# Performance work log

Measured on AMD Instinct MI355X. Metric: run time of the kernel, lower is better.

Reference implementation:

```python
import jax, jax.numpy as jnp
import numpy as np

NUM_HEADS = 16
HEAD_DIM = 64  # d_model // num_heads = 1024 // 16
NUM_BUCKETS = 20


def setup_inputs() -> dict:
    key = jax.random.key(0)
    ks = jax.random.split(key, 5)
    B, S, D = 2, 2048, 1024
    v = jax.random.normal(ks[0], (B, S, D), dtype=jnp.float32)
    k = jax.random.normal(ks[1], (B, S, D), dtype=jnp.float32)
    q = jax.random.normal(ks[2], (B, S, D), dtype=jnp.float32)
    mask = jax.random.randint(ks[3], (B, S, S), 0, 2).astype(jnp.bool_)
    diff_matrix = jax.random.randint(ks[4], (B, S, S), 0, NUM_BUCKETS)
    rel_bias = jax.random.normal(jax.random.fold_in(key, 7), (NUM_BUCKETS, NUM_HEADS), dtype=jnp.float32)
    return {"v": v, "k": k, "q": q, "mask": mask, "diff_matrix": diff_matrix, "rel_bias": rel_bias}


def _split_heads(x):
    B, S, _ = x.shape
    return x.reshape(B, S, NUM_HEADS, HEAD_DIM).transpose(0, 2, 1, 3)  # [B,H,S,hd]


def reference(v, k, q, mask, diff_matrix, rel_bias):
    B, S, D = q.shape
    qh, kh, vh = _split_heads(q), _split_heads(k), _split_heads(v)
    scale = 1.0 / jnp.sqrt(jnp.float32(HEAD_DIM))
    scores = jnp.einsum('bhqd,bhkd->bhqk', qh, kh) * scale  # [B,H,S,S]
    # relative bias: gather [B,S,S,H] -> [B,H,S,S]
    bias = rel_bias[diff_matrix].transpose(0, 3, 1, 2)
    att = jax.nn.silu(scores + bias)
    att = jnp.where(mask[:, None, :, :], att, 0.0)
    av = jnp.einsum('bhqk,bhkd->bhqd', att, vh)  # [B,H,S,hd]
    return av.transpose(0, 2, 1, 3).reshape(B, S, D)
```

## Files before the change

### kernel.cpp

```cpp
#include <hip/hip_runtime.h>
#include <cstdint>
#include <cstddef>

#define SEQ 2048
#define DM 1024
#define NH 16
#define NB 20

typedef _Float16 half8 __attribute__((ext_vector_type(8)));
typedef _Float16 half4 __attribute__((ext_vector_type(4)));
typedef float f32x4 __attribute__((ext_vector_type(4)));
typedef int i32x4 __attribute__((ext_vector_type(4)));
typedef unsigned int u32;
typedef unsigned int u32x2 __attribute__((ext_vector_type(2)));

#define KF_HALVES 4194304
#define VF_HALVES 4194304

__global__ __launch_bounds__(256) void pa_prep(
    const float* __restrict__ v, const float* __restrict__ k,
    const int* __restrict__ diff, const int* __restrict__ mask,
    _Float16* __restrict__ KF, _Float16* __restrict__ VF,
    unsigned char* __restrict__ PB) {
  const int bid = blockIdx.x, tid = threadIdx.x;
  if (bid < 2048) {
    int img = bid >> 4;
    int bb = img >> 6, kt = img & 63;
    int tix = ((bid & 15) << 8) | tid;
    int r = tix >> 7;
    int c0 = (tix & 127) << 3;
    const float* src = k + ((size_t)(bb * SEQ + kt * 32 + r)) * DM + c0;
    f32x4 a = *(const f32x4*)src;
    f32x4 c = *(const f32x4*)(src + 4);
    half8 o = {(_Float16)a[0], (_Float16)a[1], (_Float16)a[2], (_Float16)a[3],
               (_Float16)c[0], (_Float16)c[1], (_Float16)c[2], (_Float16)c[3]};
    int h = c0 >> 6, dh = (c0 >> 5) & 1, g4 = (c0 >> 3) & 3;
    int k2 = r >> 4, l16 = r & 15;
    int lane = g4 * 16 + l16;
    size_t off = ((size_t)((bb * 16 + h) * 64 + kt)) * 2048 + (k2 * 2 + dh) * 512 + lane * 8;
    *(half8*)(KF + off) = o;
  } else if (bid < 3072) {
    int b3 = bid - 2048;
    int img = b3 >> 3;
    int bb = img >> 6, kt = img & 63;
    int tix = ((b3 & 7) << 8) | tid;
    int kq = tix >> 8;
    int k2 = kq >> 2, g4 = kq & 3;
    int d0 = (tix & 255) << 2;
    const float* src = v + ((size_t)(bb * SEQ + kt * 32 + k2 * 16 + g4 * 4)) * DM + d0;
    f32x4 m0 = *(const f32x4*)(src);
    f32x4 m1 = *(const f32x4*)(src + DM);
    f32x4 m2 = *(const f32x4*)(src + 2 * DM);
    f32x4 m3 = *(const f32x4*)(src + 3 * DM);
#pragma unroll
    for (int i = 0; i < 4; ++i) {
      int d = d0 + i;
      int l16 = d & 15, dt = (d >> 4) & 3, dtp = dt >> 1, w = dt & 1, h = d >> 6;
      int lane = g4 * 16 + l16;
      half4 o = {(_Float16)m0[i], (_Float16)m1[i], (_Float16)m2[i], (_Float16)m3[i]};
      size_t off = ((size_t)((bb * 16 + h) * 64 + kt)) * 2048 + (k2 * 2 + dtp) * 512 + lane * 8 + w * 4;
      *(half4*)(VF + off) = o;
    }
  } else {
    int b4 = bid - 3072;
    int job = b4 >> 5;
    int bb = job >> 6, qblk = job & 63;
    int tix = ((b4 & 31) << 8) | tid;
    int kt = tix >> 7;
    int rem = tix & 127;
    int g4 = rem & 3, l16 = (rem >> 2) & 15, qs = rem >> 6;
    int lane = g4 * 16 + l16;
    int qrow = qblk * 32 + qs * 16 + l16;
    size_t rowbase = ((size_t)(bb * SEQ + qrow)) * SEQ;
    u32x2 wds;
#pragma unroll
    for (int k2 = 0; k2 < 2; ++k2) {
      int kk = kt * 32 + k2 * 16 + g4 * 4;
      i32x4 dv = *(const i32x4*)(diff + rowbase + kk);
      i32x4 mv = *(const i32x4*)(mask + rowbase + kk);
      u32 wd = 0;
#pragma unroll
      for (int r = 0; r < 4; ++r) {
        u32 byte = mv[r] ? (u32)dv[r] : 20u;
        wd |= byte << (8 * r);
      }
      wds[k2] = wd;
    }
    size_t off = ((size_t)job) * 65536 + (size_t)(kt * 2 + qs) * 512 + lane * 8;
    *(u32x2*)(PB + off) = wds;
  }
}

__global__ __launch_bounds__(256, 4) void pa_main(
    const _Float16* __restrict__ KF, const _Float16* __restrict__ VF,
    const unsigned char* __restrict__ PB, const float* __restrict__ q,
    const float* __restrict__ relbias, float* __restrict__ out) {
  const int tid = threadIdx.x, lane = tid & 63, wid = tid >> 6;
  const int l16 = lane & 15, g4 = lane >> 4;
  const int bid = blockIdx.x;
  const int g = bid & 7;
  const int b = g >> 2, ksp = (g >> 1) & 1, hh = g & 1;
  const int rid = bid >> 3;
  const int qblk = rid & 63, hq = rid >> 6;
  const int h = hh * 8 + hq * 4 + wid;
  const int qbase = qblk * 32;

  float rbv = -30000.f;
  if (lane < NB) rbv = relbias[lane * NH + h];
  const int rbi = __float_as_int(rbv);

  half8 qf[2][2];
#pragma unroll
  for (int qs = 0; qs < 2; ++qs)
#pragma unroll
    for (int dh = 0; dh < 2; ++dh) {
      const float* s = q + ((size_t)(b * SEQ + qbase + qs * 16 + l16)) * DM + h * 64 + dh * 32 + g4 * 8;
      f32x4 a = *(const f32x4*)s;
      f32x4 c = *(const f32x4*)(s + 4);
      qf[qs][dh] = {(_Float16)a[0], (_Float16)a[1], (_Float16)a[2], (_Float16)a[3],
                    (_Float16)c[0], (_Float16)c[1], (_Float16)c[2], (_Float16)c[3]};
    }

  const f32x4 zf = {0.f, 0.f, 0.f, 0.f};
  f32x4 acc[2][4];
#pragma unroll
  for (int qs = 0; qs < 2; ++qs)
#pragma unroll
    for (int dt = 0; dt < 4; ++dt) acc[qs][dt] = zf;

  const _Float16* kfb = KF + ((size_t)((b * 16 + h) * 64 + ksp * 32)) * 2048 + lane * 8;
  const _Float16* vfb = VF + ((size_t)((b * 16 + h) * 64 + ksp * 32)) * 2048 + lane * 8;
  const unsigned char* pbb = PB + ((size_t)(b * 64 + qblk)) * 65536 + (size_t)(ksp * 32) * 1024 + lane * 8;

  for (int t = 0; t < 32; ++t) {
    half8 kf[2][2], vv[2][2];
#pragma unroll
    for (int k2 = 0; k2 < 2; ++k2)
#pragma unroll
      for (int j = 0; j < 2; ++j) {
        kf[k2][j] = *(const half8*)(kfb + (k2 * 2 + j) * 512);
        vv[k2][j] = *(const half8*)(vfb + (k2 * 2 + j) * 512);
      }
    u32x2 pbw[2];
    pbw[0] = *(const u32x2*)(pbb);
    pbw[1] = *(const u32x2*)(pbb + 512);

#pragma unroll
    for (int k2 = 0; k2 < 2; ++k2) {
      f32x4 sa[2];
#pragma unroll
      for (int qs = 0; qs < 2; ++qs) {
        sa[qs] = __builtin_amdgcn_mfma_f32_16x16x32_f16(kf[k2][0], qf[qs][0], zf, 0, 0, 0);
        sa[qs] = __builtin_amdgcn_mfma_f32_16x16x32_f16(kf[k2][1], qf[qs][1], sa[qs], 0, 0, 0);
      }
      half4 pf[2];
#pragma unroll
      for (int qs = 0; qs < 2; ++qs) {
        u32 u = pbw[qs][k2];
#pragma unroll
        for (int r = 0; r < 4; ++r) {
          int idx = (int)(((u >> (8 * r)) & 0xffu) << 2);
          float bias = __int_as_float(__builtin_amdgcn_ds_bpermute(idx, rbi));
          float x = fmaf(sa[qs][r], 0.125f, bias);
          float e = __expf(-x);
          float y = x * __builtin_amdgcn_rcpf(1.0f + e);
          pf[qs][r] = (_Float16)y;
        }
      }
      half4 vf0 = __builtin_shufflevector(vv[k2][0], vv[k2][0], 0, 1, 2, 3);
      half4 vf1 = __builtin_shufflevector(vv[k2][0], vv[k2][0], 4, 5, 6, 7);
      half4 vf2 = __builtin_shufflevector(vv[k2][1], vv[k2][1], 0, 1, 2, 3);
      half4 vf3 = __builtin_shufflevector(vv[k2][1], vv[k2][1], 4, 5, 6, 7);
#pragma unroll
      for (int qs = 0; qs < 2; ++qs) {
        acc[qs][0] = __builtin_amdgcn_mfma_f32_16x16x16f16(pf[qs], vf0, acc[qs][0], 0, 0, 0);
        acc[qs][1] = __builtin_amdgcn_mfma_f32_16x16x16f16(pf[qs], vf1, acc[qs][1], 0, 0, 0);
        acc[qs][2] = __builtin_amdgcn_mfma_f32_16x16x16f16(pf[qs], vf2, acc[qs][2], 0, 0, 0);
        acc[qs][3] = __builtin_amdgcn_mfma_f32_16x16x16f16(pf[qs], vf3, acc[qs][3], 0, 0, 0);
      }
    }
    kfb += 2048; vfb += 2048; pbb += 1024;
  }

#pragma unroll
  for (int qs = 0; qs < 2; ++qs)
#pragma unroll
    for (int dt = 0; dt < 4; ++dt)
#pragma unroll
      for (int r = 0; r < 4; ++r) {
        int qrow = qbase + qs * 16 + g4 * 4 + r;
        int d = h * 64 + dt * 16 + l16;
        atomicAdd(&out[((size_t)(b * SEQ) + qrow) * DM + d], acc[qs][dt][r]);
      }
}

extern "C" void kernel_launch(void* const* d_in, const int* in_sizes, int n_in,
                              void* d_out, int out_size, void* d_ws, size_t ws_size,
                              hipStream_t stream) {
  const float* v = (const float*)d_in[0];
  const float* k = (const float*)d_in[1];
  const float* q = (const float*)d_in[2];
  const int* mask = (const int*)d_in[3];
  const int* diff = (const int*)d_in[4];
  const float* relbias = (const float*)d_in[5];
  float* out = (float*)d_out;

  _Float16* KF = (_Float16*)d_ws;
  _Float16* VF = KF + KF_HALVES;
  unsigned char* PB = (unsigned char*)(VF + VF_HALVES);
  if (ws_size < (size_t)25165824) return;

  hipMemsetAsync(d_out, 0, (size_t)out_size * sizeof(float), stream);
  pa_prep<<<7168, 256, 0, stream>>>(v, k, diff, mask, KF, VF, PB);
  pa_main<<<1024, 256, 0, stream>>>(KF, VF, PB, q, relbias, out);
}
```

Before: 108.3 us.

## Compute SiLU in packed fp16, fold scale into Q, remap blocks and pack bias bytes

The SiLU epilogue now runs in packed half2 arithmetic (exp2, rcp) instead of per-element fp32 expf and rcp. The 1/8 score scale is folded into Q at load time, and the bias indices are pre-shifted in the prep kernel so the lane-permute needs no shift. The bias-byte layout is changed so each lane loads 16 bytes in one access. Blocks are remapped so the four waves in a block share a head and work on different query blocks, improving K/V reuse across waves, and the loop is unrolled by 2. The fp16 SiLU loses precision and can overflow or underflow for large scores.

```diff
diff --git a/kernel.cpp b/kernel.cpp
--- a/kernel.cpp
+++ b/kernel.cpp
@@ -1,4 +1,5 @@
 #include <hip/hip_runtime.h>
+#include <hip/hip_fp16.h>
 #include <cstdint>
 #include <cstddef>
 
@@ -9,6 +10,7 @@
 
 typedef _Float16 half8 __attribute__((ext_vector_type(8)));
 typedef _Float16 half4 __attribute__((ext_vector_type(4)));
+typedef _Float16 h2v __attribute__((ext_vector_type(2)));
 typedef float f32x4 __attribute__((ext_vector_type(4)));
 typedef int i32x4 __attribute__((ext_vector_type(4)));
 typedef unsigned int u32;
@@ -81,14 +83,34 @@
       u32 wd = 0;
 #pragma unroll
       for (int r = 0; r < 4; ++r) {
-        u32 byte = mv[r] ? (u32)dv[r] : 20u;
+        u32 byte = mv[r] ? ((u32)dv[r] << 2) : 80u;
         wd |= byte << (8 * r);
       }
       wds[k2] = wd;
     }
-    size_t off = ((size_t)job) * 65536 + (size_t)(kt * 2 + qs) * 512 + lane * 8;
+    size_t off = ((size_t)job) * 65536 + (size_t)kt * 1024 + (size_t)lane * 16 + (size_t)qs * 8;
     *(u32x2*)(PB + off) = wds;
   }
+}
+
+__device__ __forceinline__ half4 silu4(const f32x4& s, u32 u, int rbi) {
+  float b0 = __int_as_float(__builtin_amdgcn_ds_bpermute((int)(u & 0xffu), rbi));
+  float b1 = __int_as_float(__builtin_amdgcn_ds_bpermute((int)((u >> 8) & 0xffu), rbi));
+  float b2 = __int_as_float(__builtin_amdgcn_ds_bpermute((int)((u >> 16) & 0xffu), rbi));
+  float b3 = __int_as_float(__builtin_amdgcn_ds_bpermute((int)(u >> 24), rbi));
+  h2v x01 = __builtin_bit_cast(h2v, __builtin_amdgcn_cvt_pkrtz(s[0], s[1])) +
+            __builtin_bit_cast(h2v, __builtin_amdgcn_cvt_pkrtz(b0, b1));
+  h2v x23 = __builtin_bit_cast(h2v, __builtin_amdgcn_cvt_pkrtz(s[2], s[3])) +
+            __builtin_bit_cast(h2v, __builtin_amdgcn_cvt_pkrtz(b2, b3));
+  const h2v NL2E = {(_Float16)-1.44269504f, (_Float16)-1.44269504f};
+  const h2v ONE = {(_Float16)1.0f, (_Float16)1.0f};
+  h2v m01 = x01 * NL2E, m23 = x23 * NL2E;
+  h2v e01 = __builtin_bit_cast(h2v, h2exp2(__builtin_bit_cast(__half2, m01)));
+  h2v e23 = __builtin_bit_cast(h2v, h2exp2(__builtin_bit_cast(__half2, m23)));
+  h2v d01 = e01 + ONE, d23 = e23 + ONE;
+  h2v y01 = x01 * __builtin_bit_cast(h2v, h2rcp(__builtin_bit_cast(__half2, d01)));
+  h2v y23 = x23 * __builtin_bit_cast(h2v, h2rcp(__builtin_bit_cast(__half2, d23)));
+  return (half4){y01[0], y01[1], y23[0], y23[1]};
 }
 
 __global__ __launch_bounds__(256, 4) void pa_main(
@@ -97,16 +119,15 @@
     const float* __restrict__ relbias, float* __restrict__ out) {
   const int tid = threadIdx.x, lane = tid & 63, wid = tid >> 6;
   const int l16 = lane & 15, g4 = lane >> 4;
-  const int bid = blockIdx.x;
-  const int g = bid & 7;
-  const int b = g >> 2, ksp = (g >> 1) & 1, hh = g & 1;
-  const int rid = bid >> 3;
-  const int qblk = rid & 63, hq = rid >> 6;
-  const int h = hh * 8 + hq * 4 + wid;
+  const int L = (blockIdx.x & 7) * 128 + (blockIdx.x >> 3);
+  const int h = L & 15;
+  const int qgrp = (L >> 4) & 15;
+  const int ksp = (L >> 8) & 1;
+  const int b = L >> 9;
+  const int qblk = qgrp * 4 + wid;
   const int qbase = qblk * 32;
 
-  float rbv = -30000.f;
-  if (lane < NB) rbv = relbias[lane * NH + h];
+  const float rbv = (lane < NB) ? relbias[lane * NH + h] : -30000.0f;
   const int rbi = __float_as_int(rbv);
 
   half8 qf[2][2];
@@ -117,8 +138,10 @@
       const float* s = q + ((size_t)(b * SEQ + qbase + qs * 16 + l16)) * DM + h * 64 + dh * 32 + g4 * 8;
       f32x4 a = *(const f32x4*)s;
       f32x4 c = *(const f32x4*)(s + 4);
-      qf[qs][dh] = {(_Float16)a[0], (_Float16)a[1], (_Float16)a[2], (_Float16)a[3],
-                    (_Float16)c[0], (_Float16)c[1], (_Float16)c[2], (_Float16)c[3]};
+      qf[qs][dh] = {(_Float16)(a[0] * 0.125f), (_Float16)(a[1] * 0.125f),
+                    (_Float16)(a[2] * 0.125f), (_Float16)(a[3] * 0.125f),
+                    (_Float16)(c[0] * 0.125f), (_Float16)(c[1] * 0.125f),
+                    (_Float16)(c[2] * 0.125f), (_Float16)(c[3] * 0.125f)};
     }
 
   const f32x4 zf = {0.f, 0.f, 0.f, 0.f};
@@ -130,47 +153,34 @@
 
   const _Float16* kfb = KF + ((size_t)((b * 16 + h) * 64 + ksp * 32)) * 2048 + lane * 8;
   const _Float16* vfb = VF + ((size_t)((b * 16 + h) * 64 + ksp * 32)) * 2048 + lane * 8;
-  const unsigned char* pbb = PB + ((size_t)(b * 64 + qblk)) * 65536 + (size_t)(ksp * 32) * 1024 + lane * 8;
-
+  const unsigned char* pbb = PB + ((size_t)(b * 64 + qblk)) * 65536 + (size_t)(ksp * 32) * 1024 + lane * 16;
+
+#pragma unroll 2
   for (int t = 0; t < 32; ++t) {
-    half8 kf[2][2], vv[2][2];
-#pragma unroll
-    for (int k2 = 0; k2 < 2; ++k2)
-#pragma unroll
-      for (int j = 0; j < 2; ++j) {
-        kf[k2][j] = *(const half8*)(kfb + (k2 * 2 + j) * 512);
-        vv[k2][j] = *(const half8*)(vfb + (k2 * 2 + j) * 512);
-      }
-    u32x2 pbw[2];
-    pbw[0] = *(const u32x2*)(pbb);
-    pbw[1] = *(const u32x2*)(pbb + 512);
+    half8 kfr[4], vvr[4];
+#pragma unroll
+    for (int j = 0; j < 4; ++j) {
+      kfr[j] = *(const half8*)(kfb + (size_t)t * 2048 + j * 512);
+      vvr[j] = *(const half8*)(vfb + (size_t)t * 2048 + j * 512);
+    }
+    i32x4 pq = *(const i32x4*)(pbb + (size_t)t * 1024);
 
 #pragma unroll
     for (int k2 = 0; k2 < 2; ++k2) {
       f32x4 sa[2];
 #pragma unroll
       for (int qs = 0; qs < 2; ++qs) {
-        sa[qs] = __builtin_amdgcn_mfma_f32_16x16x32_f16(kf[k2][0], qf[qs][0], zf, 0, 0, 0);
-        sa[qs] = __builtin_amdgcn_mfma_f32_16x16x32_f16(kf[k2][1], qf[qs][1], sa[qs], 0, 0, 0);
+        sa[qs] = __builtin_amdgcn_mfma_f32_16x16x32_f16(kfr[k2 * 2 + 0], qf[qs][0], zf, 0, 0, 0);
+        sa[qs] = __builtin_amdgcn_mfma_f32_16x16x32_f16(kfr[k2 * 2 + 1], qf[qs][1], sa[qs], 0, 0, 0);
       }
       half4 pf[2];
-#pragma unroll
-      for (int qs = 0; qs < 2; ++qs) {
-        u32 u = pbw[qs][k2];
-#pragma unroll
-        for (int r = 0; r < 4; ++r) {
-          int idx = (int)(((u >> (8 * r)) & 0xffu) << 2);
-          float bias = __int_as_float(__builtin_amdgcn_ds_bpermute(idx, rbi));
-          float x = fmaf(sa[qs][r], 0.125f, bias);
-          float e = __expf(-x);
-          float y = x * __builtin_amdgcn_rcpf(1.0f + e);
-          pf[qs][r] = (_Float16)y;
-        }
-      }
-      half4 vf0 = __builtin_shufflevector(vv[k2][0], vv[k2][0], 0, 1, 2, 3);
-      half4 vf1 = __builtin_shufflevector(vv[k2][0], vv[k2][0], 4, 5, 6, 7);
-      half4 vf2 = __builtin_shufflevector(vv[k2][1], vv[k2][1], 0, 1, 2, 3);
-      half4 vf3 = __builtin_shufflevector(vv[k2][1], vv[k2][1], 4, 5, 6, 7);
+      pf[0] = silu4(sa[0], (u32)pq[k2], rbi);
+      pf[1] = silu4(sa[1], (u32)pq[2 + k2], rbi);
+
+      half4 vf0 = __builtin_shufflevector(vvr[k2 * 2 + 0], vvr[k2 * 2 + 0], 0, 1, 2, 3);
+      half4 vf1 = __builtin_shufflevector(vvr[k2 * 2 + 0], vvr[k2 * 2 + 0], 4, 5, 6, 7);
+      half4 vf2 = __builtin_shufflevector(vvr[k2 * 2 + 1], vvr[k2 * 2 + 1], 0, 1, 2, 3);
+      half4 vf3 = __builtin_shufflevector(vvr[k2 * 2 + 1], vvr[k2 * 2 + 1], 4, 5, 6, 7);
 #pragma unroll
       for (int qs = 0; qs < 2; ++qs) {
         acc[qs][0] = __builtin_amdgcn_mfma_f32_16x16x16f16(pf[qs], vf0, acc[qs][0], 0, 0, 0);
@@ -179,7 +189,6 @@
         acc[qs][3] = __builtin_amdgcn_mfma_f32_16x16x16f16(pf[qs], vf3, acc[qs][3], 0, 0, 0);
       }
     }
-    kfb += 2048; vfb += 2048; pbb += 1024;
   }
 
 #pragma unroll
@@ -210,7 +219,7 @@
   unsigned char* PB = (unsigned char*)(VF + VF_HALVES);
   if (ws_size < (size_t)25165824) return;
 
-  hipMemsetAsync(d_out, 0, (size_t)out_size * sizeof(float), stream);
+  (void)hipMemsetAsync(d_out, 0, (size_t)out_size * sizeof(float), stream);
   pa_prep<<<7168, 256, 0, stream>>>(v, k, diff, mask, KF, VF, PB);
   pa_main<<<1024, 256, 0, stream>>>(KF, VF, PB, q, relbias, out);
 }
```

Measured after the change: 105.8 us. -2.3%, faster.
